# Kernel optimization log

Hardware: AMD Instinct MI355X
Metric: run time of the kernel (lower is better)

Reference implementation:

```python
import jax, jax.numpy as jnp
import numpy as np

B, T, N, H, D = 4, 512, 4, 8, 64
FACTOR = 5


def setup_inputs() -> dict:
    key = jax.random.key(0)
    k1, k2, k3, k4 = jax.random.split(key, 4)
    queries = jax.random.normal(k1, (B, T, N, H, D), dtype=jnp.float32)
    keys = jax.random.normal(k2, (B, T, N, H, D), dtype=jnp.float32)
    values = jax.random.normal(k3, (B, T, N, H, D), dtype=jnp.float32)
    sample_k = min(FACTOR * int(np.ceil(np.log(T))), T)  # = 35
    index_sample = jax.random.randint(k4, (T, sample_k), 0, T)
    return {"queries": queries, "keys": keys, "values": values,
            "index_sample": index_sample}


def _merge_heads(x):
    # [B, T, N, H, D] -> [B, H, T, N*D]  (matches transpose(3,2).reshape.transpose(2,1))
    b, t, n, h, d = x.shape
    return jnp.transpose(x, (0, 1, 3, 2, 4)).reshape(b, t, h, n * d).transpose(0, 2, 1, 3)


def reference(queries, keys, values, index_sample):
    b, t, n, h, d = queries.shape
    e = n * d
    Q = _merge_heads(queries)   # [B, H, T, E]
    K = _merge_heads(keys)
    V = _merge_heads(values)
    u = index_sample.shape[1]   # sample_k == n_top == factor*ceil(ln T)

    # --- _prob_QK: sampled QK scores, sparsity measure, top-u query select ---
    K_sample = K[:, :, index_sample, :]                      # [B, H, T, u, E]
    QK_sample = jnp.einsum('bhte,bhtse->bhts', Q, K_sample)  # [B, H, T, u]
    M = QK_sample.max(axis=-1) - QK_sample.sum(axis=-1) / t  # [B, H, T]
    _, M_top = jax.lax.top_k(M, u)                           # [B, H, u]
    Q_reduce = jnp.take_along_axis(Q, M_top[..., None], axis=2)  # [B, H, u, E]
    scores = jnp.einsum('bhue,bhte->bhut', Q_reduce, K)      # [B, H, u, T]

    # scale uses 1/sqrt(d_k) of the ORIGINAL query last dim (D), not N*D
    scores = scores * (1.0 / jnp.sqrt(jnp.asarray(d, scores.dtype)))

    # --- initial context (mask_flag=False): mean of V broadcast over T ---
    context = jnp.broadcast_to(V.mean(axis=2, keepdims=True), (b, h, t, e))

    # --- update context at selected query positions ---
    attn = jax.nn.softmax(scores, axis=-1)                   # [B, H, u, T]
    update = jnp.einsum('bhut,bhte->bhue', attn, V)          # [B, H, u, E]
    bi = jnp.arange(b)[:, None, None]
    hi = jnp.arange(h)[None, :, None]
    context = context.at[bi, hi, M_top].set(update)          # scatter-write

    # [B, H, T, E] -> [B, T, N, H, D]
    out = context.transpose(0, 2, 1, 3).reshape(b, t, h, n, d).transpose(0, 1, 3, 2, 4)
    return out
```

## Files before the change

### kernel.cpp

```cpp
#include <hip/hip_runtime.h>
#include <stdint.h>

#define BB 4
#define TT 512
#define NN 4
#define HH 8
#define DD 64
#define EE 256
#define ROWS 2048
#define UPAD 36
#define NCH 8
#define CH 64


__global__ void vmean_part_kernel(const float* __restrict__ v,
                                  float* __restrict__ vpart) {
    int blk = blockIdx.x;
    int chunk = blk & 7;
    int bh = blk >> 3;
    int b = bh >> 3, h = bh & 7;
    int e = threadIdx.x;
    int n = e >> 6, d = e & 63;
    size_t base = (size_t)b * TT * ROWS + (size_t)(n * HH + h) * DD + d;
    float acc = 0.f;
    int t0 = chunk * 64;
    for (int t = t0; t < t0 + 64; ++t)
        acc += v[base + (size_t)t * ROWS];
    vpart[blk * EE + e] = acc;
}

__global__ void fill_kernel(const float* __restrict__ vmean,
                            float* __restrict__ out) {
    size_t tid4 = ((size_t)blockIdx.x * 256 + threadIdx.x) << 2;
    int d = tid4 & 63;
    size_t rest = tid4 >> 6;
    int h = rest & 7;  rest >>= 3;
    int n = rest & 3;  rest >>= 2;
    int b = (int)(rest >> 9);
    int e = (n << 6) + d;
    int bh = (b << 3) + h;
    float4 val = *(const float4*)(vmean + (size_t)bh * EE + e);
    *(float4*)(out + tid4) = val;
}

__global__ void m_kernel(const float* __restrict__ q,
                         const float* __restrict__ k,
                         const int* __restrict__ idx,
                         float* __restrict__ M, int U) {
    int wave = threadIdx.x >> 6, lane = threadIdx.x & 63;
    int xcd = blockIdx.x & 7;
    int bh = (xcd << 2) | ((blockIdx.x >> 3) & 3);
    int t = ((blockIdx.x >> 5) << 2) + wave;
    int r = (bh << 9) + t;
    int b = bh >> 3, h = bh & 7;
    int g = lane >> 4, x = lane & 15;
    int n = x >> 2;
    int dbase = ((x & 3) << 4);
    size_t colbase = (size_t)(n * HH + h) * DD + dbase;
    size_t qrow = ((size_t)(b * TT + t)) * ROWS + colbase;
    float4 qv0 = *(const float4*)(q + qrow);
    float4 qv1 = *(const float4*)(q + qrow + 4);
    float4 qv2 = *(const float4*)(q + qrow + 8);
    float4 qv3 = *(const float4*)(q + qrow + 12);
    float mx = -3.4e38f, sm = 0.f;
    int NB = (U + 3) >> 2;
    for (int bs = 0; bs < NB; ++bs) {
        int s = (bs << 2) + g;
        int valid = s < U;
        int sc = valid ? s : (U - 1);
        int kt = idx[t * U + sc] & (TT - 1);
        size_t krow = ((size_t)(b * TT + kt)) * ROWS + colbase;
        float4 kv0 = *(const float4*)(k + krow);
        float4 kv1 = *(const float4*)(k + krow + 4);
        float4 kv2 = *(const float4*)(k + krow + 8);
        float4 kv3 = *(const float4*)(k + krow + 12);
        float dot = qv0.x * kv0.x + qv0.y * kv0.y + qv0.z * kv0.z + qv0.w * kv0.w
                  + qv1.x * kv1.x + qv1.y * kv1.y + qv1.z * kv1.z + qv1.w * kv1.w
                  + qv2.x * kv2.x + qv2.y * kv2.y + qv2.z * kv2.z + qv2.w * kv2.w
                  + qv3.x * kv3.x + qv3.y * kv3.y + qv3.z * kv3.z + qv3.w * kv3.w;
        #pragma unroll
        for (int off = 1; off < 16; off <<= 1)
            dot += __shfl_xor(dot, off, 64);
        if (valid) { mx = fmaxf(mx, dot); sm += dot; }
    }
    mx = fmaxf(mx, __shfl_xor(mx, 16, 64));
    mx = fmaxf(mx, __shfl_xor(mx, 32, 64));
    sm += __shfl_xor(sm, 16, 64);
    sm += __shfl_xor(sm, 32, 64);
    if (lane == 0) M[r] = mx - sm * (1.0f / TT);
}

__global__ void topk_kernel(const float* __restrict__ M,
                            int* __restrict__ Mtop,
                            const float* __restrict__ vpart,
                            float* __restrict__ vmean, int U) {
    __shared__ float sM[TT];
    int bh = blockIdx.x;
    int t = threadIdx.x;
    sM[t] = M[bh * TT + t];
    if (t < 64) Mtop[bh * 64 + t] = 0;
    if (t < EE) {
        float acc = 0.f;
        #pragma unroll
        for (int c = 0; c < 8; ++c)
            acc += vpart[(bh * 8 + c) * EE + t];
        vmean[bh * EE + t] = acc * (1.0f / TT);
    }
    __syncthreads();
    float mv = sM[t];
    int rank = 0;
    for (int i = 0; i < TT; ++i) {
        float o = sM[i];
        rank += (o > mv) || (o == mv && i < t);
    }
    if (rank < U) Mtop[bh * 64 + rank] = t;
}

__global__ __launch_bounds__(256)
void attn_partial(const float* __restrict__ q, const float* __restrict__ k,
                  const float* __restrict__ v, const int* __restrict__ Mtop,
                  float* __restrict__ Opart, float* __restrict__ ml, int U) {
    __shared__ float qs[UPAD * 130];
    __shared__ float Bs[CH * 132];
    __shared__ float S[UPAD * 68];

    int bx = blockIdx.x;
    int bh = bx >> 3, ch = bx & 7;
    int b = bh >> 3, h = bh & 7;
    int tid = threadIdx.x;
    int wv = tid >> 6, l = tid & 63;

    float acc[4][4];
    #pragma unroll
    for (int i = 0; i < 4; ++i)
        #pragma unroll
        for (int j = 0; j < 4; ++j) acc[i][j] = 0.f;

    for (int h2 = 0; h2 < 2; ++h2) {
        int eb = h2 * 128;
        for (int u = wv; u < UPAD; u += 4) {
            int uu = (u < U) ? u : (U - 1);
            int qt = Mtop[bh * 64 + uu] & (TT - 1);
            size_t rowq = ((size_t)(b * TT + qt)) * ROWS;
            #pragma unroll
            for (int j = 0; j < 2; ++j) {
                int e = eb + l + 64 * j;
                qs[u * 130 + l + 64 * j] = q[rowq + (size_t)((e >> 6) * HH + h) * DD + (e & 63)];
            }
        }
        for (int r = wv; r < CH; r += 4) {
            size_t rowk = ((size_t)(b * TT + ch * CH + r)) * ROWS;
            #pragma unroll
            for (int j = 0; j < 2; ++j) {
                int e = eb + l + 64 * j;
                Bs[r * 129 + l + 64 * j] = k[rowk + (size_t)((e >> 6) * HH + h) * DD + (e & 63)];
            }
        }
        __syncthreads();
        if (tid < 144) {
            int ug = tid >> 4, tg = tid & 15;
            int u0 = ug << 2, t0 = tg << 2;
            for (int e = 0; e < 128; ++e) {
                float kx0 = Bs[(t0 + 0) * 129 + e];
                float kx1 = Bs[(t0 + 1) * 129 + e];
                float kx2 = Bs[(t0 + 2) * 129 + e];
                float kx3 = Bs[(t0 + 3) * 129 + e];
                #pragma unroll
                for (int i = 0; i < 4; ++i) {
                    float qv = qs[(u0 + i) * 130 + e];
                    acc[i][0] += qv * kx0;
                    acc[i][1] += qv * kx1;
                    acc[i][2] += qv * kx2;
                    acc[i][3] += qv * kx3;
                }
            }
        }
        __syncthreads();
    }
    if (tid < 144) {
        int ug = tid >> 4, tg = tid & 15;
        int u0 = ug << 2, t0 = tg << 2;
        #pragma unroll
        for (int i = 0; i < 4; ++i)
            #pragma unroll
            for (int j = 0; j < 4; ++j)
                S[(u0 + i) * 68 + t0 + j] = acc[i][j] * 0.125f;
    }
    __syncthreads();

    if (tid < UPAD) {
        float m = -3.4e38f;
        for (int t = 0; t < CH; ++t) m = fmaxf(m, S[tid * 68 + t]);
        float lsum = 0.f;
        for (int t = 0; t < CH; ++t) {
            float p = __expf(S[tid * 68 + t] - m);
            S[tid * 68 + t] = p;
            lsum += p;
        }
        size_t mli = ((size_t)(bh * NCH + ch) * UPAD + tid) * 2;
        ml[mli] = m;
        ml[mli + 1] = lsum;
    }
    __syncthreads();

    int ugp = tid >> 5, el = tid & 31;
    int u0p = ugp * 5;
    for (int vh = 0; vh < 2; ++vh) {
        for (int r = wv; r < CH; r += 4) {
            size_t rowv = ((size_t)(b * TT + ch * CH + r)) * ROWS;
            #pragma unroll
            for (int j = 0; j < 2; ++j) {
                int e = vh * 128 + l + 64 * j;
                Bs[r * 132 + l + 64 * j] = v[rowv + (size_t)((e >> 6) * HH + h) * DD + (e & 63)];
            }
        }
        __syncthreads();
        float4 o[5];
        #pragma unroll
        for (int i = 0; i < 5; ++i) o[i] = make_float4(0.f, 0.f, 0.f, 0.f);
        for (int t = 0; t < CH; ++t) {
            float4 v4 = *(const float4*)&Bs[t * 132 + 4 * el];
            #pragma unroll
            for (int i = 0; i < 5; ++i) {
                int uc = u0p + i; if (uc > 35) uc = 35;
                float p = S[uc * 68 + t];
                o[i].x += p * v4.x; o[i].y += p * v4.y;
                o[i].z += p * v4.z; o[i].w += p * v4.w;
            }
        }
        #pragma unroll
        for (int i = 0; i < 5; ++i) {
            int u = u0p + i;
            if (u < UPAD)
                *(float4*)&Opart[((size_t)(bh * NCH + ch) * UPAD + u) * EE + vh * 128 + 4 * el] = o[i];
        }
        __syncthreads();
    }
}

__global__ void combine_kernel(const float* __restrict__ Opart,
                               const float* __restrict__ ml,
                               const int* __restrict__ Mtop,
                               float* __restrict__ out, int U) {
    int bx = blockIdx.x;
    int bh = bx / U, ui = bx % U;
    int b = bh >> 3, h = bh & 7;
    int el = threadIdx.x;
    float mc[NCH], lc[NCH];
    float gm = -3.4e38f;
    #pragma unroll
    for (int c = 0; c < NCH; ++c) {
        size_t mli = ((size_t)(bh * NCH + c) * UPAD + ui) * 2;
        mc[c] = ml[mli]; lc[c] = ml[mli + 1];
        gm = fmaxf(gm, mc[c]);
    }
    float L = 0.f;
    float fc[NCH];
    #pragma unroll
    for (int c = 0; c < NCH; ++c) { fc[c] = __expf(mc[c] - gm); L += lc[c] * fc[c]; }
    float inv = 1.0f / L;
    float4 a = make_float4(0.f, 0.f, 0.f, 0.f);
    #pragma unroll
    for (int c = 0; c < NCH; ++c) {
        float4 o = *(const float4*)&Opart[((size_t)(bh * NCH + c) * UPAD + ui) * EE + 4 * el];
        a.x += fc[c] * o.x; a.y += fc[c] * o.y;
        a.z += fc[c] * o.z; a.w += fc[c] * o.w;
    }
    int qt = Mtop[bh * 64 + ui] & (TT - 1);
    int e0 = 4 * el, n = el >> 4;
    size_t ooff = ((size_t)(b * TT + qt)) * ROWS + (size_t)(n * HH + h) * DD + (e0 & 63);
    a.x *= inv; a.y *= inv; a.z *= inv; a.w *= inv;
    *(float4*)(out + ooff) = a;
}


__global__ __launch_bounds__(1024)
void vmean_kernel(const float* __restrict__ v, float* __restrict__ vmean) {
    __shared__ float part[4][EE];
    int bh = blockIdx.x;
    int b = bh >> 3, h = bh & 7;
    int e = threadIdx.x & 255;
    int chunk = threadIdx.x >> 8;
    int n = e >> 6, d = e & 63;
    size_t base = (size_t)b * TT * ROWS + (size_t)(n * HH + h) * DD + d;
    float acc = 0.f;
    int t0 = chunk * 128;
    for (int t = t0; t < t0 + 128; ++t)
        acc += v[base + (size_t)t * ROWS];
    part[chunk][e] = acc;
    __syncthreads();
    if (threadIdx.x < EE)
        vmean[bh * EE + threadIdx.x] =
            (part[0][threadIdx.x] + part[1][threadIdx.x] +
             part[2][threadIdx.x] + part[3][threadIdx.x]) * (1.0f / TT);
}

__global__ void topk_only_kernel(const float* __restrict__ M,
                                 int* __restrict__ Mtop, int U) {
    __shared__ float sM[TT];
    int bh = blockIdx.x;
    int t = threadIdx.x;
    sM[t] = M[bh * TT + t];
    if (t < 64) Mtop[bh * 64 + t] = 0;
    __syncthreads();
    float mv = sM[t];
    int rank = 0;
    for (int i = 0; i < TT; ++i) {
        float o = sM[i];
        rank += (o > mv) || (o == mv && i < t);
    }
    if (rank < U) Mtop[bh * 64 + rank] = t;
}

__global__ void update_kernel(const float* __restrict__ q,
                              const float* __restrict__ k,
                              const float* __restrict__ v,
                              const int* __restrict__ Mtop,
                              float* __restrict__ out, int U) {
    __shared__ float qs[EE];
    __shared__ float sc[TT];
    __shared__ float red[256];
    int blk = blockIdx.x;
    int ui = blk % U;
    int bh = blk / U;
    int b = bh >> 3, h = bh & 7;
    int tid = threadIdx.x;
    int qt = Mtop[bh * 64 + ui] & (TT - 1);
    {
        int n = tid >> 6, d = tid & 63;
        qs[tid] = q[((size_t)(b * TT + qt)) * ROWS + (size_t)(n * HH + h) * DD + d];
    }
    __syncthreads();
    #pragma unroll
    for (int rep = 0; rep < 2; ++rep) {
        int t = tid + rep * 256;
        size_t kb = ((size_t)(b * TT + t)) * ROWS + (size_t)h * DD;
        float acc = 0.f;
        #pragma unroll
        for (int n = 0; n < NN; ++n) {
            const float* kn = k + kb + (size_t)n * HH * DD;
            #pragma unroll 4
            for (int d4 = 0; d4 < DD; d4 += 4) {
                float4 kv = *(const float4*)(kn + d4);
                int e = n * 64 + d4;
                acc += qs[e] * kv.x + qs[e + 1] * kv.y + qs[e + 2] * kv.z + qs[e + 3] * kv.w;
            }
        }
        sc[t] = acc * 0.125f;
    }
    __syncthreads();
    red[tid] = fmaxf(sc[tid], sc[tid + 256]);
    __syncthreads();
    for (int s = 128; s > 0; s >>= 1) {
        if (tid < s) red[tid] = fmaxf(red[tid], red[tid + s]);
        __syncthreads();
    }
    float mx = red[0];
    __syncthreads();
    float e0 = __expf(sc[tid] - mx);
    float e1 = __expf(sc[tid + 256] - mx);
    sc[tid] = e0; sc[tid + 256] = e1;
    red[tid] = e0 + e1;
    __syncthreads();
    for (int s = 128; s > 0; s >>= 1) {
        if (tid < s) red[tid] += red[tid + s];
        __syncthreads();
    }
    float inv = 1.0f / red[0];
    __syncthreads();
    {
        int n = tid >> 6, d = tid & 63;
        size_t vb = (size_t)b * TT * ROWS + (size_t)(n * HH + h) * DD + d;
        float acc = 0.f;
        for (int t = 0; t < TT; ++t)
            acc += sc[t] * v[vb + (size_t)t * ROWS];
        out[((size_t)(b * TT + qt)) * ROWS + (size_t)(n * HH + h) * DD + d] = acc * inv;
    }
}

__global__ __launch_bounds__(1024)
void fused_probattn(const float* __restrict__ qp, const float* __restrict__ kp,
                    const float* __restrict__ vp, const int* __restrict__ idx,
                    float* __restrict__ out, int U) {
    __shared__ float vmean[EE];
    __shared__ float M[TT];
    __shared__ float sc[TT];
    __shared__ float qs[EE];
    __shared__ float red[64];
    __shared__ int   Mtop[64];
    const int bh = blockIdx.x;
    const int b = bh >> 3, h = bh & 7;
    const int tid = threadIdx.x;
    const int wave = tid >> 6, lane = tid & 63;
    if (tid < EE) {
        int n = tid >> 6, d = tid & 63;
        size_t base = (size_t)b * TT * ROWS + (size_t)(n * HH + h) * DD + d;
        float acc = 0.f;
        for (int t = 0; t < TT; ++t) acc += vp[base + (size_t)t * ROWS];
        vmean[tid] = acc * (1.0f / TT);
    }
    __syncthreads();
    for (int i = tid; i < TT * EE; i += 1024) {
        int t = i >> 8, e = i & 255;
        int n = e >> 6, d = e & 63;
        out[((size_t)(b * TT + t)) * ROWS + (size_t)(n * HH + h) * DD + d] = vmean[e];
    }
    {
        int e = lane << 2;
        int n = e >> 6, d = e & 63;
        size_t ebase = (size_t)(n * HH + h) * DD + d;
        for (int t = wave; t < TT; t += 16) {
            float4 qv = *(const float4*)(qp + ((size_t)(b * TT + t)) * ROWS + ebase);
            float mx = -3.4e38f, sm = 0.f;
            for (int s = 0; s < U; ++s) {
                int kt = idx[t * U + s] & (TT - 1);
                float4 kv = *(const float4*)(kp + ((size_t)(b * TT + kt)) * ROWS + ebase);
                float dot = qv.x * kv.x + qv.y * kv.y + qv.z * kv.z + qv.w * kv.w;
                #pragma unroll
                for (int off = 32; off; off >>= 1) dot += __shfl_xor(dot, off, 64);
                mx = fmaxf(mx, dot);
                sm += dot;
            }
            if (lane == 0) M[t] = mx - sm * (1.0f / TT);
        }
    }
    __syncthreads();
    if (tid < 64) Mtop[tid] = 0;
    __syncthreads();
    if (tid < TT) {
        float mv = M[tid];
        int rank = 0;
        for (int i = 0; i < TT; ++i) {
            float o = M[i];
            rank += (o > mv) || (o == mv && i < tid);
        }
        if (rank < U) Mtop[rank] = tid;
    }
    __syncthreads();
    for (int ui = 0; ui < U; ++ui) {
        int qt = Mtop[ui];
        if (tid < EE) {
            int n = tid >> 6, d = tid & 63;
            qs[tid] = qp[((size_t)(b * TT + qt)) * ROWS + (size_t)(n * HH + h) * DD + d];
        }
        __syncthreads();
        if (tid < TT) {
            float acc = 0.f;
            size_t kb = ((size_t)(b * TT + tid)) * ROWS + (size_t)h * DD;
            for (int n = 0; n < NN; ++n) {
                const float* kn = kp + kb + (size_t)n * HH * DD;
                for (int d = 0; d < DD; ++d) acc += qs[n * 64 + d] * kn[d];
            }
            sc[tid] = acc * 0.125f;
        }
        __syncthreads();
        float val = (tid < TT) ? sc[tid] : -3.4e38f;
        #pragma unroll
        for (int off = 32; off; off >>= 1) val = fmaxf(val, __shfl_xor(val, off, 64));
        if (lane == 0) red[wave] = val;
        __syncthreads();
        if (tid == 0) {
            float m = red[0];
            for (int w = 1; w < 16; ++w) m = fmaxf(m, red[w]);
            red[32] = m;
        }
        __syncthreads();
        float mx = red[32];
        float ev = 0.f;
        if (tid < TT) { ev = __expf(sc[tid] - mx); sc[tid] = ev; }
        __syncthreads();
        float sv = ev;
        #pragma unroll
        for (int off = 32; off; off >>= 1) sv += __shfl_xor(sv, off, 64);
        if (lane == 0) red[wave] = sv;
        __syncthreads();
        if (tid == 0) {
            float s = 0.f;
            for (int w = 0; w < 16; ++w) s += red[w];
            red[32] = s;
        }
        __syncthreads();
        float inv = 1.0f / red[32];
        if (tid < EE) {
            int n = tid >> 6, d = tid & 63;
            size_t vb = (size_t)b * TT * ROWS + (size_t)(n * HH + h) * DD + d;
            float acc = 0.f;
            for (int t = 0; t < TT; ++t) acc += sc[t] * vp[vb + (size_t)t * ROWS];
            out[((size_t)(b * TT + qt)) * ROWS + (size_t)(n * HH + h) * DD + d] = acc * inv;
        }
        __syncthreads();
    }
}

extern "C" void kernel_launch(void* const* d_in, const int* in_sizes, int n_in,
                              void* d_out, int out_size, void* d_ws, size_t ws_size,
                              hipStream_t stream) {
    const float* q = (const float*)d_in[0];
    const float* k = (const float*)d_in[1];
    const float* v = (const float*)d_in[2];
    const int* idx = (const int*)d_in[3];
    float* out = (float*)d_out;
    int U = in_sizes[3] / TT;

    const size_t NEED_FLASH = 204800 + (size_t)32 * NCH * UPAD * EE * 4 + 1024;
    const size_t NEED_MID = 160 * 1024;
    char* ws = (char*)d_ws;
    float* M     = (float*)(ws);
    int*   Mtop  = (int*)  (ws + 65536);
    float* vmean = (float*)(ws + 98304);
    float* ml    = (float*)(ws + 131072);
    float* Opart = (float*)(ws + 204800);
    float* vpart = (float*)(ws + 204800);

    if (ws_size >= NEED_FLASH && U == 35) {
        vmean_part_kernel<<<BB * HH * 8, 256, 0, stream>>>(v, vpart);
        m_kernel<<<BB * HH * TT / 4, 256, 0, stream>>>(q, k, idx, M, U);
        topk_kernel<<<BB * HH, TT, 0, stream>>>(M, Mtop, vpart, vmean, U);
        fill_kernel<<<4096, 256, 0, stream>>>(vmean, out);
        attn_partial<<<BB * HH * NCH, 256, 0, stream>>>(q, k, v, Mtop, Opart, ml, U);
        combine_kernel<<<BB * HH * U, 64, 0, stream>>>(Opart, ml, Mtop, out, U);
    } else if (ws_size >= NEED_MID) {
        vmean_kernel<<<BB * HH, 1024, 0, stream>>>(v, vmean);
        fill_kernel<<<4096, 256, 0, stream>>>(vmean, out);
        m_kernel<<<BB * HH * TT / 4, 256, 0, stream>>>(q, k, idx, M, U);
        topk_only_kernel<<<BB * HH, TT, 0, stream>>>(M, Mtop, U);
        update_kernel<<<BB * HH * U, 256, 0, stream>>>(q, k, v, Mtop, out, U);
    } else {
        fused_probattn<<<BB * HH, 1024, 0, stream>>>(q, k, v, idx, out, U);
    }
}
```

Baseline: 186.8 us.

## Merge vmean into M kernel and fill into attention kernel to cut launches

Fuses the V-mean partial-sum blocks into the sampled-QK sparsity kernel as extra blocks, and folds the output fill into the attention-partial kernel as extra blocks, which cuts the fast path from six launches to four. The M computation also stages sampled indices in shared memory and double-buffers the K-row loads so each iteration's gather overlaps the previous dot product. The aim is to remove launch gaps and gather latency. In exchange, heterogeneous blocks share one kernel's register and LDS budget, so the fill blocks reserve the attention kernel's large static shared memory, which can limit occupancy.

Result: no change. 186.5 us (-0.1%).

```diff
diff --git a/kernel.cpp b/kernel.cpp
--- a/kernel.cpp
+++ b/kernel.cpp
@@ -13,20 +13,293 @@
 #define CH 64
 
 
-__global__ void vmean_part_kernel(const float* __restrict__ v,
-                                  float* __restrict__ vpart) {
-    int blk = blockIdx.x;
-    int chunk = blk & 7;
-    int bh = blk >> 3;
+__global__ __launch_bounds__(256)
+void m_vmean_kernel(const float* __restrict__ q, const float* __restrict__ k,
+                    const float* __restrict__ v, const int* __restrict__ idx,
+                    float* __restrict__ M, float* __restrict__ vpart, int U) {
+    if (blockIdx.x >= 4096) {
+        int blk = blockIdx.x - 4096;
+        int chunk = blk & 7, bh = blk >> 3;
+        int b = bh >> 3, h = bh & 7;
+        int e = threadIdx.x;
+        int n = e >> 6, d = e & 63;
+        size_t base = (size_t)b * TT * ROWS + (size_t)(n * HH + h) * DD + d;
+        float acc = 0.f;
+        int t0 = chunk * 64;
+        for (int t = t0; t < t0 + 64; ++t)
+            acc += v[base + (size_t)t * ROWS];
+        vpart[blk * EE + e] = acc;
+        return;
+    }
+    __shared__ int sidx[4][40];
+    int wave = threadIdx.x >> 6, lane = threadIdx.x & 63;
+    int xcd = blockIdx.x & 7;
+    int bh = (xcd << 2) | ((blockIdx.x >> 3) & 3);
+    int t = ((blockIdx.x >> 5) << 2) + wave;
     int b = bh >> 3, h = bh & 7;
-    int e = threadIdx.x;
+    if (lane < U) sidx[wave][lane] = idx[t * U + lane] & (TT - 1);
+    int g = lane >> 4, x = lane & 15;
+    int n = x >> 2;
+    int dbase = (x & 3) << 4;
+    size_t colbase = (size_t)(n * HH + h) * DD + dbase;
+    const float* qr = q + ((size_t)(b * TT + t)) * ROWS + colbase;
+    float4 qv0 = *(const float4*)qr;
+    float4 qv1 = *(const float4*)(qr + 4);
+    float4 qv2 = *(const float4*)(qr + 8);
+    float4 qv3 = *(const float4*)(qr + 12);
+    float mx = -3.4e38f, sm = 0.f;
+    const int NB = (U + 3) >> 2;
+    int sP = g; if (sP >= U) sP = U - 1;
+    const float* kr = k + ((size_t)(b * TT + sidx[wave][sP])) * ROWS + colbase;
+    float4 c0 = *(const float4*)kr,       c1 = *(const float4*)(kr + 4),
+           c2 = *(const float4*)(kr + 8), c3 = *(const float4*)(kr + 12);
+    for (int bs = 0; bs < NB; ++bs) {
+        int sn = ((bs + 1) << 2) + g;
+        if (sn >= U) sn = U - 1;
+        const float* krn = k + ((size_t)(b * TT + sidx[wave][sn])) * ROWS + colbase;
+        float4 n0 = *(const float4*)krn,       n1 = *(const float4*)(krn + 4),
+               n2 = *(const float4*)(krn + 8), n3 = *(const float4*)(krn + 12);
+        float dot = qv0.x * c0.x + qv0.y * c0.y + qv0.z * c0.z + qv0.w * c0.w
+                  + qv1.x * c1.x + qv1.y * c1.y + qv1.z * c1.z + qv1.w * c1.w
+                  + qv2.x * c2.x + qv2.y * c2.y + qv2.z * c2.z + qv2.w * c2.w
+                  + qv3.x * c3.x + qv3.y * c3.y + qv3.z * c3.z + qv3.w * c3.w;
+        #pragma unroll
+        for (int off = 1; off < 16; off <<= 1)
+            dot += __shfl_xor(dot, off, 64);
+        int s = (bs << 2) + g;
+        if (s < U) { mx = fmaxf(mx, dot); sm += dot; }
+        c0 = n0; c1 = n1; c2 = n2; c3 = n3;
+    }
+    mx = fmaxf(mx, __shfl_xor(mx, 16, 64));
+    mx = fmaxf(mx, __shfl_xor(mx, 32, 64));
+    sm += __shfl_xor(sm, 16, 64);
+    sm += __shfl_xor(sm, 32, 64);
+    if (lane == 0) M[(bh << 9) + t] = mx - sm * (1.0f / TT);
+}
+
+__global__ void topk_kernel(const float* __restrict__ M,
+                            int* __restrict__ Mtop,
+                            const float* __restrict__ vpart,
+                            float* __restrict__ vmean, int U) {
+    __shared__ float sM[TT];
+    int bh = blockIdx.x;
+    int t = threadIdx.x;
+    sM[t] = M[bh * TT + t];
+    if (t < 64) Mtop[bh * 64 + t] = 0;
+    if (t < EE) {
+        float acc = 0.f;
+        #pragma unroll
+        for (int c = 0; c < 8; ++c)
+            acc += vpart[(bh * 8 + c) * EE + t];
+        vmean[bh * EE + t] = acc * (1.0f / TT);
+    }
+    __syncthreads();
+    float mv = sM[t];
+    int rank = 0;
+    for (int i = 0; i < TT; ++i) {
+        float o = sM[i];
+        rank += (o > mv) || (o == mv && i < t);
+    }
+    if (rank < U) Mtop[bh * 64 + rank] = t;
+}
+
+__global__ __launch_bounds__(256)
+void attn_fill(const float* __restrict__ q, const float* __restrict__ k,
+               const float* __restrict__ v, const int* __restrict__ Mtop,
+               const float* __restrict__ vmean, float* __restrict__ out,
+               float* __restrict__ Opart, float* __restrict__ ml, int U) {
+    __shared__ float qs[UPAD * 130];
+    __shared__ float Bs[CH * 132];
+    __shared__ float S[UPAD * 68];
+
+    if (blockIdx.x >= 256) {
+        int fb = blockIdx.x - 256;
+        size_t i0 = (size_t)fb * 256 + threadIdx.x;
+        #pragma unroll
+        for (int r = 0; r < 8; ++r) {
+            size_t tid4 = (i0 + (size_t)r * 131072) << 2;
+            int d = tid4 & 63;
+            size_t rest = tid4 >> 6;
+            int h = rest & 7;  rest >>= 3;
+            int nn = rest & 3; rest >>= 2;
+            int b = (int)(rest >> 9);
+            int e = (nn << 6) + d;
+            int bh = (b << 3) + h;
+            float4 val = *(const float4*)(vmean + (size_t)bh * EE + e);
+            *(float4*)(out + tid4) = val;
+        }
+        return;
+    }
+
+    int bx = blockIdx.x;
+    int bh = bx >> 3, ch = bx & 7;
+    int b = bh >> 3, h = bh & 7;
+    int tid = threadIdx.x;
+    int wv = tid >> 6, l = tid & 63;
+
+    float acc[4][4];
+    #pragma unroll
+    for (int i = 0; i < 4; ++i)
+        #pragma unroll
+        for (int j = 0; j < 4; ++j) acc[i][j] = 0.f;
+
+    for (int h2 = 0; h2 < 2; ++h2) {
+        int eb = h2 * 128;
+        for (int u = wv; u < UPAD; u += 4) {
+            int uu = (u < U) ? u : (U - 1);
+            int qt = Mtop[bh * 64 + uu] & (TT - 1);
+            size_t rowq = ((size_t)(b * TT + qt)) * ROWS;
+            #pragma unroll
+            for (int j = 0; j < 2; ++j) {
+                int e = eb + l + 64 * j;
+                qs[u * 130 + l + 64 * j] = q[rowq + (size_t)((e >> 6) * HH + h) * DD + (e & 63)];
+            }
+        }
+        for (int r = wv; r < CH; r += 4) {
+            size_t rowk = ((size_t)(b * TT + ch * CH + r)) * ROWS;
+            #pragma unroll
+            for (int j = 0; j < 2; ++j) {
+                int e = eb + l + 64 * j;
+                Bs[r * 129 + l + 64 * j] = k[rowk + (size_t)((e >> 6) * HH + h) * DD + (e & 63)];
+            }
+        }
+        __syncthreads();
+        if (tid < 144) {
+            int ug = tid >> 4, tg = tid & 15;
+            int u0 = ug << 2, t0 = tg << 2;
+            for (int e = 0; e < 128; ++e) {
+                float kx0 = Bs[(t0 + 0) * 129 + e];
+                float kx1 = Bs[(t0 + 1) * 129 + e];
+                float kx2 = Bs[(t0 + 2) * 129 + e];
+                float kx3 = Bs[(t0 + 3) * 129 + e];
+                #pragma unroll
+                for (int i = 0; i < 4; ++i) {
+                    float qv = qs[(u0 + i) * 130 + e];
+                    acc[i][0] += qv * kx0;
+                    acc[i][1] += qv * kx1;
+                    acc[i][2] += qv * kx2;
+                    acc[i][3] += qv * kx3;
+                }
+            }
+        }
+        __syncthreads();
+    }
+    if (tid < 144) {
+        int ug = tid >> 4, tg = tid & 15;
+        int u0 = ug << 2, t0 = tg << 2;
+        #pragma unroll
+        for (int i = 0; i < 4; ++i)
+            #pragma unroll
+            for (int j = 0; j < 4; ++j)
+                S[(u0 + i) * 68 + t0 + j] = acc[i][j] * 0.125f;
+    }
+    __syncthreads();
+
+    if (tid < UPAD) {
+        float m = -3.4e38f;
+        for (int t = 0; t < CH; ++t) m = fmaxf(m, S[tid * 68 + t]);
+        float lsum = 0.f;
+        for (int t = 0; t < CH; ++t) {
+            float p = __expf(S[tid * 68 + t] - m);
+            S[tid * 68 + t] = p;
+            lsum += p;
+        }
+        size_t mli = ((size_t)(bh * NCH + ch) * UPAD + tid) * 2;
+        ml[mli] = m;
+        ml[mli + 1] = lsum;
+    }
+    __syncthreads();
+
+    int ugp = tid >> 5, el = tid & 31;
+    int u0p = ugp * 5;
+    for (int vh = 0; vh < 2; ++vh) {
+        for (int r = wv; r < CH; r += 4) {
+            size_t rowv = ((size_t)(b * TT + ch * CH + r)) * ROWS;
+            #pragma unroll
+            for (int j = 0; j < 2; ++j) {
+                int e = vh * 128 + l + 64 * j;
+                Bs[r * 132 + l + 64 * j] = v[rowv + (size_t)((e >> 6) * HH + h) * DD + (e & 63)];
+            }
+        }
+        __syncthreads();
+        float4 o[5];
+        #pragma unroll
+        for (int i = 0; i < 5; ++i) o[i] = make_float4(0.f, 0.f, 0.f, 0.f);
+        for (int t = 0; t < CH; ++t) {
+            float4 v4 = *(const float4*)&Bs[t * 132 + 4 * el];
+            #pragma unroll
+            for (int i = 0; i < 5; ++i) {
+                int uc = u0p + i; if (uc > 35) uc = 35;
+                float p = S[uc * 68 + t];
+                o[i].x += p * v4.x; o[i].y += p * v4.y;
+                o[i].z += p * v4.z; o[i].w += p * v4.w;
+            }
+        }
+        #pragma unroll
+        for (int i = 0; i < 5; ++i) {
+            int u = u0p + i;
+            if (u < UPAD)
+                *(float4*)&Opart[((size_t)(bh * NCH + ch) * UPAD + u) * EE + vh * 128 + 4 * el] = o[i];
+        }
+        __syncthreads();
+    }
+}
+
+__global__ void combine_kernel(const float* __restrict__ Opart,
+                               const float* __restrict__ ml,
+                               const int* __restrict__ Mtop,
+                               float* __restrict__ out, int U) {
+    int bx = blockIdx.x;
+    int bh = bx / U, ui = bx % U;
+    int b = bh >> 3, h = bh & 7;
+    int el = threadIdx.x;
+    float mc[NCH], lc[NCH];
+    float gm = -3.4e38f;
+    #pragma unroll
+    for (int c = 0; c < NCH; ++c) {
+        size_t mli = ((size_t)(bh * NCH + c) * UPAD + ui) * 2;
+        mc[c] = ml[mli]; lc[c] = ml[mli + 1];
+        gm = fmaxf(gm, mc[c]);
+    }
+    float L = 0.f;
+    float fc[NCH];
+    #pragma unroll
+    for (int c = 0; c < NCH; ++c) { fc[c] = __expf(mc[c] - gm); L += lc[c] * fc[c]; }
+    float inv = 1.0f / L;
+    float4 a = make_float4(0.f, 0.f, 0.f, 0.f);
+    #pragma unroll
+    for (int c = 0; c < NCH; ++c) {
+        float4 o = *(const float4*)&Opart[((size_t)(bh * NCH + c) * UPAD + ui) * EE + 4 * el];
+        a.x += fc[c] * o.x; a.y += fc[c] * o.y;
+        a.z += fc[c] * o.z; a.w += fc[c] * o.w;
+    }
+    int qt = Mtop[bh * 64 + ui] & (TT - 1);
+    int e0 = 4 * el, n = el >> 4;
+    size_t ooff = ((size_t)(b * TT + qt)) * ROWS + (size_t)(n * HH + h) * DD + (e0 & 63);
+    a.x *= inv; a.y *= inv; a.z *= inv; a.w *= inv;
+    *(float4*)(out + ooff) = a;
+}
+
+
+__global__ __launch_bounds__(1024)
+void vmean_kernel(const float* __restrict__ v, float* __restrict__ vmean) {
+    __shared__ float part[4][EE];
+    int bh = blockIdx.x;
+    int b = bh >> 3, h = bh & 7;
+    int e = threadIdx.x & 255;
+    int chunk = threadIdx.x >> 8;
     int n = e >> 6, d = e & 63;
     size_t base = (size_t)b * TT * ROWS + (size_t)(n * HH + h) * DD + d;
     float acc = 0.f;
-    int t0 = chunk * 64;
-    for (int t = t0; t < t0 + 64; ++t)
+    int t0 = chunk * 128;
+    for (int t = t0; t < t0 + 128; ++t)
         acc += v[base + (size_t)t * ROWS];
-    vpart[blk * EE + e] = acc;
+    part[chunk][e] = acc;
+    __syncthreads();
+    if (threadIdx.x < EE)
+        vmean[bh * EE + threadIdx.x] =
+            (part[0][threadIdx.x] + part[1][threadIdx.x] +
+             part[2][threadIdx.x] + part[3][threadIdx.x]) * (1.0f / TT);
 }
 
 __global__ void fill_kernel(const float* __restrict__ vmean,
@@ -43,19 +316,18 @@
     *(float4*)(out + tid4) = val;
 }
 
-__global__ void m_kernel(const float* __restrict__ q,
-                         const float* __restrict__ k,
-                         const int* __restrict__ idx,
-                         float* __restrict__ M, int U) {
+__global__ void m_only_kernel(const float* __restrict__ q,
+                              const float* __restrict__ k,
+                              const int* __restrict__ idx,
+                              float* __restrict__ M, int U) {
     int wave = threadIdx.x >> 6, lane = threadIdx.x & 63;
-    int xcd = blockIdx.x & 7;
-    int bh = (xcd << 2) | ((blockIdx.x >> 3) & 3);
-    int t = ((blockIdx.x >> 5) << 2) + wave;
-    int r = (bh << 9) + t;
+    int r = (blockIdx.x << 2) + wave;
+    int t = r & (TT - 1);
+    int bh = r >> 9;
     int b = bh >> 3, h = bh & 7;
     int g = lane >> 4, x = lane & 15;
     int n = x >> 2;
-    int dbase = ((x & 3) << 4);
+    int dbase = (x & 3) << 4;
     size_t colbase = (size_t)(n * HH + h) * DD + dbase;
     size_t qrow = ((size_t)(b * TT + t)) * ROWS + colbase;
     float4 qv0 = *(const float4*)(q + qrow);
@@ -90,211 +362,6 @@
     if (lane == 0) M[r] = mx - sm * (1.0f / TT);
 }
 
-__global__ void topk_kernel(const float* __restrict__ M,
-                            int* __restrict__ Mtop,
-                            const float* __restrict__ vpart,
-                            float* __restrict__ vmean, int U) {
-    __shared__ float sM[TT];
-    int bh = blockIdx.x;
-    int t = threadIdx.x;
-    sM[t] = M[bh * TT + t];
-    if (t < 64) Mtop[bh * 64 + t] = 0;
-    if (t < EE) {
-        float acc = 0.f;
-        #pragma unroll
-        for (int c = 0; c < 8; ++c)
-            acc += vpart[(bh * 8 + c) * EE + t];
-        vmean[bh * EE + t] = acc * (1.0f / TT);
-    }
-    __syncthreads();
-    float mv = sM[t];
-    int rank = 0;
-    for (int i = 0; i < TT; ++i) {
-        float o = sM[i];
-        rank += (o > mv) || (o == mv && i < t);
-    }
-    if (rank < U) Mtop[bh * 64 + rank] = t;
-}
-
-__global__ __launch_bounds__(256)
-void attn_partial(const float* __restrict__ q, const float* __restrict__ k,
-                  const float* __restrict__ v, const int* __restrict__ Mtop,
-                  float* __restrict__ Opart, float* __restrict__ ml, int U) {
-    __shared__ float qs[UPAD * 130];
-    __shared__ float Bs[CH * 132];
-    __shared__ float S[UPAD * 68];
-
-    int bx = blockIdx.x;
-    int bh = bx >> 3, ch = bx & 7;
-    int b = bh >> 3, h = bh & 7;
-    int tid = threadIdx.x;
-    int wv = tid >> 6, l = tid & 63;
-
-    float acc[4][4];
-    #pragma unroll
-    for (int i = 0; i < 4; ++i)
-        #pragma unroll
-        for (int j = 0; j < 4; ++j) acc[i][j] = 0.f;
-
-    for (int h2 = 0; h2 < 2; ++h2) {
-        int eb = h2 * 128;
-        for (int u = wv; u < UPAD; u += 4) {
-            int uu = (u < U) ? u : (U - 1);
-            int qt = Mtop[bh * 64 + uu] & (TT - 1);
-            size_t rowq = ((size_t)(b * TT + qt)) * ROWS;
-            #pragma unroll
-            for (int j = 0; j < 2; ++j) {
-                int e = eb + l + 64 * j;
-                qs[u * 130 + l + 64 * j] = q[rowq + (size_t)((e >> 6) * HH + h) * DD + (e & 63)];
-            }
-        }
-        for (int r = wv; r < CH; r += 4) {
-            size_t rowk = ((size_t)(b * TT + ch * CH + r)) * ROWS;
-            #pragma unroll
-            for (int j = 0; j < 2; ++j) {
-                int e = eb + l + 64 * j;
-                Bs[r * 129 + l + 64 * j] = k[rowk + (size_t)((e >> 6) * HH + h) * DD + (e & 63)];
-            }
-        }
-        __syncthreads();
-        if (tid < 144) {
-            int ug = tid >> 4, tg = tid & 15;
-            int u0 = ug << 2, t0 = tg << 2;
-            for (int e = 0; e < 128; ++e) {
-                float kx0 = Bs[(t0 + 0) * 129 + e];
-                float kx1 = Bs[(t0 + 1) * 129 + e];
-                float kx2 = Bs[(t0 + 2) * 129 + e];
-                float kx3 = Bs[(t0 + 3) * 129 + e];
-                #pragma unroll
-                for (int i = 0; i < 4; ++i) {
-                    float qv = qs[(u0 + i) * 130 + e];
-                    acc[i][0] += qv * kx0;
-                    acc[i][1] += qv * kx1;
-                    acc[i][2] += qv * kx2;
-                    acc[i][3] += qv * kx3;
-                }
-            }
-        }
-        __syncthreads();
-    }
-    if (tid < 144) {
-        int ug = tid >> 4, tg = tid & 15;
-        int u0 = ug << 2, t0 = tg << 2;
-        #pragma unroll
-        for (int i = 0; i < 4; ++i)
-            #pragma unroll
-            for (int j = 0; j < 4; ++j)
-                S[(u0 + i) * 68 + t0 + j] = acc[i][j] * 0.125f;
-    }
-    __syncthreads();
-
-    if (tid < UPAD) {
-        float m = -3.4e38f;
-        for (int t = 0; t < CH; ++t) m = fmaxf(m, S[tid * 68 + t]);
-        float lsum = 0.f;
-        for (int t = 0; t < CH; ++t) {
-            float p = __expf(S[tid * 68 + t] - m);
-            S[tid * 68 + t] = p;
-            lsum += p;
-        }
-        size_t mli = ((size_t)(bh * NCH + ch) * UPAD + tid) * 2;
-        ml[mli] = m;
-        ml[mli + 1] = lsum;
-    }
-    __syncthreads();
-
-    int ugp = tid >> 5, el = tid & 31;
-    int u0p = ugp * 5;
-    for (int vh = 0; vh < 2; ++vh) {
-        for (int r = wv; r < CH; r += 4) {
-            size_t rowv = ((size_t)(b * TT + ch * CH + r)) * ROWS;
-            #pragma unroll
-            for (int j = 0; j < 2; ++j) {
-                int e = vh * 128 + l + 64 * j;
-                Bs[r * 132 + l + 64 * j] = v[rowv + (size_t)((e >> 6) * HH + h) * DD + (e & 63)];
-            }
-        }
-        __syncthreads();
-        float4 o[5];
-        #pragma unroll
-        for (int i = 0; i < 5; ++i) o[i] = make_float4(0.f, 0.f, 0.f, 0.f);
-        for (int t = 0; t < CH; ++t) {
-            float4 v4 = *(const float4*)&Bs[t * 132 + 4 * el];
-            #pragma unroll
-            for (int i = 0; i < 5; ++i) {
-                int uc = u0p + i; if (uc > 35) uc = 35;
-                float p = S[uc * 68 + t];
-                o[i].x += p * v4.x; o[i].y += p * v4.y;
-                o[i].z += p * v4.z; o[i].w += p * v4.w;
-            }
-        }
-        #pragma unroll
-        for (int i = 0; i < 5; ++i) {
-            int u = u0p + i;
-            if (u < UPAD)
-                *(float4*)&Opart[((size_t)(bh * NCH + ch) * UPAD + u) * EE + vh * 128 + 4 * el] = o[i];
-        }
-        __syncthreads();
-    }
-}
-
-__global__ void combine_kernel(const float* __restrict__ Opart,
-                               const float* __restrict__ ml,
-                               const int* __restrict__ Mtop,
-                               float* __restrict__ out, int U) {
-    int bx = blockIdx.x;
-    int bh = bx / U, ui = bx % U;
-    int b = bh >> 3, h = bh & 7;
-    int el = threadIdx.x;
-    float mc[NCH], lc[NCH];
-    float gm = -3.4e38f;
-    #pragma unroll
-    for (int c = 0; c < NCH; ++c) {
-        size_t mli = ((size_t)(bh * NCH + c) * UPAD + ui) * 2;
-        mc[c] = ml[mli]; lc[c] = ml[mli + 1];
-        gm = fmaxf(gm, mc[c]);
-    }
-    float L = 0.f;
-    float fc[NCH];
-    #pragma unroll
-    for (int c = 0; c < NCH; ++c) { fc[c] = __expf(mc[c] - gm); L += lc[c] * fc[c]; }
-    float inv = 1.0f / L;
-    float4 a = make_float4(0.f, 0.f, 0.f, 0.f);
-    #pragma unroll
-    for (int c = 0; c < NCH; ++c) {
-        float4 o = *(const float4*)&Opart[((size_t)(bh * NCH + c) * UPAD + ui) * EE + 4 * el];
-        a.x += fc[c] * o.x; a.y += fc[c] * o.y;
-        a.z += fc[c] * o.z; a.w += fc[c] * o.w;
-    }
-    int qt = Mtop[bh * 64 + ui] & (TT - 1);
-    int e0 = 4 * el, n = el >> 4;
-    size_t ooff = ((size_t)(b * TT + qt)) * ROWS + (size_t)(n * HH + h) * DD + (e0 & 63);
-    a.x *= inv; a.y *= inv; a.z *= inv; a.w *= inv;
-    *(float4*)(out + ooff) = a;
-}
-
-
-__global__ __launch_bounds__(1024)
-void vmean_kernel(const float* __restrict__ v, float* __restrict__ vmean) {
-    __shared__ float part[4][EE];
-    int bh = blockIdx.x;
-    int b = bh >> 3, h = bh & 7;
-    int e = threadIdx.x & 255;
-    int chunk = threadIdx.x >> 8;
-    int n = e >> 6, d = e & 63;
-    size_t base = (size_t)b * TT * ROWS + (size_t)(n * HH + h) * DD + d;
-    float acc = 0.f;
-    int t0 = chunk * 128;
-    for (int t = t0; t < t0 + 128; ++t)
-        acc += v[base + (size_t)t * ROWS];
-    part[chunk][e] = acc;
-    __syncthreads();
-    if (threadIdx.x < EE)
-        vmean[bh * EE + threadIdx.x] =
-            (part[0][threadIdx.x] + part[1][threadIdx.x] +
-             part[2][threadIdx.x] + part[3][threadIdx.x]) * (1.0f / TT);
-}
-
 __global__ void topk_only_kernel(const float* __restrict__ M,
                                  int* __restrict__ Mtop, int U) {
     __shared__ float sM[TT];
@@ -513,16 +580,14 @@
     float* vpart = (float*)(ws + 204800);
 
     if (ws_size >= NEED_FLASH && U == 35) {
-        vmean_part_kernel<<<BB * HH * 8, 256, 0, stream>>>(v, vpart);
-        m_kernel<<<BB * HH * TT / 4, 256, 0, stream>>>(q, k, idx, M, U);
+        m_vmean_kernel<<<4096 + 256, 256, 0, stream>>>(q, k, v, idx, M, vpart, U);
         topk_kernel<<<BB * HH, TT, 0, stream>>>(M, Mtop, vpart, vmean, U);
-        fill_kernel<<<4096, 256, 0, stream>>>(vmean, out);
-        attn_partial<<<BB * HH * NCH, 256, 0, stream>>>(q, k, v, Mtop, Opart, ml, U);
+        attn_fill<<<256 + 512, 256, 0, stream>>>(q, k, v, Mtop, vmean, out, Opart, ml, U);
         combine_kernel<<<BB * HH * U, 64, 0, stream>>>(Opart, ml, Mtop, out, U);
     } else if (ws_size >= NEED_MID) {
         vmean_kernel<<<BB * HH, 1024, 0, stream>>>(v, vmean);
         fill_kernel<<<4096, 256, 0, stream>>>(vmean, out);
-        m_kernel<<<BB * HH * TT / 4, 256, 0, stream>>>(q, k, idx, M, U);
+        m_only_kernel<<<BB * HH * TT / 4, 256, 0, stream>>>(q, k, idx, M, U);
         topk_only_kernel<<<BB * HH, TT, 0, stream>>>(M, Mtop, U);
         update_kernel<<<BB * HH * U, 256, 0, stream>>>(q, k, v, Mtop, out, U);
     } else {
```
